# Kernel optimization log

Measured on AMD Instinct MI355X. Metric: run time of the kernel, lower is better.

The kernel has to match this reference:

```python
import jax, jax.numpy as jnp
import numpy as np

NUM_EMBEDDINGS = 1024
EMBEDDING_DIM = 64
COMMITMENT_COST = 0.25


def setup_inputs() -> dict:
    key = jax.random.key(0)
    k1, k2 = jax.random.split(key)
    latents = jax.random.normal(k1, (64, EMBEDDING_DIM, 32, 32), dtype=jnp.float32)
    # torch init: uniform_(-1/num_embeddings, 1/num_embeddings)
    codebook = jax.random.uniform(
        k2, (NUM_EMBEDDINGS, EMBEDDING_DIM), dtype=jnp.float32,
        minval=-1.0 / NUM_EMBEDDINGS, maxval=1.0 / NUM_EMBEDDINGS)
    return {"latents": latents, "codebook": codebook}


def reference(latents, codebook):
    B, C, H, W = latents.shape
    K = codebook.shape[0]
    x = jnp.transpose(latents, (0, 2, 3, 1))            # [B,H,W,C]
    x_flat = x.reshape(-1, C)                            # [N,C]
    # squared euclidean distances [N,K]
    dist = (jnp.sum(x_flat ** 2, axis=1, keepdims=True)
            + jnp.sum(codebook ** 2, axis=1)
            - 2.0 * x_flat @ codebook.T)
    idx = jnp.argmin(dist, axis=1)                       # [N] int
    q_flat = codebook[idx]                               # [N,C]
    q = q_flat.reshape(x.shape)                          # [B,H,W,C]
    e_loss = jnp.mean((jax.lax.stop_gradient(q) - x) ** 2)
    q_loss = jnp.mean((q - jax.lax.stop_gradient(x)) ** 2)
    vq_loss = q_loss + COMMITMENT_COST * e_loss
    # straight-through estimator
    q_st = x + jax.lax.stop_gradient(q - x)
    quantized = jnp.transpose(q_st, (0, 3, 1, 2))        # [B,C,H,W]
    # perplexity from code usage histogram
    N = x_flat.shape[0]
    avg_probs = jnp.zeros((K,), dtype=jnp.float32).at[idx].add(1.0) / N
    perplexity = jnp.exp(-jnp.sum(avg_probs * jnp.log(avg_probs + 1e-10)))
    encoding_indices = idx.reshape(B, H, W)
    return (vq_loss, quantized, perplexity, encoding_indices)
```

## Files before the change

### kernel.cpp

```cpp
#include <hip/hip_runtime.h>

#define N_PTS   65536
#define K_CODES 1024
#define C_DIM   64
#define HW      1024
#define Q_ELEMS 4194304

#define OUT_Q_OFF 1
#define OUT_P_OFF 4194305
#define OUT_I_OFF 4194306

#define WS_HIST 0
#define WS_SSE  4096
#define WS_CSUM 8192
#define WS_CBP  16384

#define EPS_A_W 7.5e-5f
#define EPS_T_W 2.0e-4f

typedef float f32x16 __attribute__((ext_vector_type(16)));
typedef short bf16x8 __attribute__((ext_vector_type(8)));

__device__ __forceinline__ unsigned short bf16rn(float f) {
    unsigned int u = __float_as_uint(f);
    return (unsigned short)((u + 0x7FFFu + ((u >> 16) & 1u)) >> 16);
}
__device__ __forceinline__ float bf16tof(unsigned short h) {
    return __uint_as_float(((unsigned int)h) << 16);
}

__device__ __forceinline__ float np_pairwise_sumsq64(const float* a) {
    float r[8];
    #pragma unroll
    for (int j = 0; j < 8; ++j) r[j] = __fmul_rn(a[j], a[j]);
    #pragma unroll
    for (int i = 8; i < 64; i += 8) {
        #pragma unroll
        for (int j = 0; j < 8; ++j)
            r[j] = __fadd_rn(r[j], __fmul_rn(a[i + j], a[i + j]));
    }
    return __fadd_rn(__fadd_rn(__fadd_rn(r[0], r[1]), __fadd_rn(r[2], r[3])),
                     __fadd_rn(__fadd_rn(r[4], r[5]), __fadd_rn(r[6], r[7])));
}

__global__ void vq_prep(const float* __restrict__ cb, float* __restrict__ csum,
                        unsigned short* __restrict__ cbp) {
    int g = blockIdx.x * 256 + threadIdx.x;
    int t = g >> 6, lane = g & 63, l31 = lane & 31, half = lane >> 5;
    int row = t * 32 + l31;
    const float* r = cb + row * 64;
    float cs = np_pairwise_sumsq64(r);
    if (half == 0) csum[row] = cs;
    size_t tb = (size_t)t * 9 * 512;
    #pragma unroll
    for (int c = 0; c < 4; ++c) {
        bf16x8 h8, l8;
        #pragma unroll
        for (int j = 0; j < 8; ++j) {
            float f = r[c * 16 + half * 8 + j];
            unsigned short h = bf16rn(f);
            h8[j] = (short)h;
            l8[j] = (short)bf16rn(f - bf16tof(h));
        }
        *(bf16x8*)(cbp + tb + (size_t)(c * 2 + 0) * 512 + lane * 8) = h8;
        *(bf16x8*)(cbp + tb + (size_t)(c * 2 + 1) * 512 + lane * 8) = l8;
    }
    bf16x8 c8;
    #pragma unroll
    for (int j = 0; j < 8; ++j) c8[j] = 0;
    if (half == 0) c8[0] = (short)bf16rn(-0.5f * cs);
    *(bf16x8*)(cbp + tb + (size_t)8 * 512 + lane * 8) = c8;
}

__global__ __launch_bounds__(256, 2) void vq_main(
        const float* __restrict__ latents,
        const float* __restrict__ cb,
        const float* __restrict__ csum,
        const unsigned short* __restrict__ cbp,
        unsigned int* __restrict__ hist,
        double* __restrict__ sse,
        float* __restrict__ out) {
    __shared__ float xs[128 * 65];
    __shared__ float tmax[32 * 128];
    __shared__ float m1f[128];
    __shared__ int   fk[128], ambig[128], acount;
    __shared__ double dred[128];

    const int tid  = threadIdx.x;
    const int lane = tid & 63, wave = tid >> 6;
    const int n0 = blockIdx.x * 128;
    const int b = n0 >> 10, hw0 = n0 & 1023;
    const float* xg = latents + (size_t)b * C_DIM * HW + hw0;

    for (int i = tid; i < 128 * 64; i += 256) {
        int p = i & 127, d = i >> 7;
        xs[p * 65 + d] = xg[(size_t)d * HW + p];
    }
    if (tid == 0) acount = 0;
    __syncthreads();

    const int l31 = lane & 31, half = lane >> 5;
    const int pb = (wave << 5) + l31;
    bf16x8 xh[4], xl[4], x4;
    #pragma unroll
    for (int c = 0; c < 4; ++c)
        #pragma unroll
        for (int j = 0; j < 8; ++j) {
            float f = xs[pb * 65 + c * 16 + half * 8 + j];
            unsigned short h = bf16rn(f);
            xh[c][j] = (short)h;
            xl[c][j] = (short)bf16rn(f - bf16tof(h));
        }
    #pragma unroll
    for (int j = 0; j < 8; ++j) x4[j] = 0;
    if (half == 0) x4[0] = (short)0x3F80;

    float m1 = -3e38f, m2 = -3e38f;
    int i1 = 0;
    const int RC[16] = {0,1,2,3,8,9,10,11,16,17,18,19,24,25,26,27};
    const int rh4 = half * 4;
    const bf16x8* base = (const bf16x8*)cbp;

    auto screen_tile = [&](int t, const bf16x8* ch, const bf16x8* cl, bf16x8 ca) {
        f32x16 accA, accB;
        #pragma unroll
        for (int r = 0; r < 16; ++r) { accA[r] = 0.0f; accB[r] = 0.0f; }
        #pragma unroll
        for (int c = 0; c < 4; ++c)
            accA = __builtin_amdgcn_mfma_f32_32x32x16_bf16(ch[c], xh[c], accA, 0, 0, 0);
        accA = __builtin_amdgcn_mfma_f32_32x32x16_bf16(ca, x4, accA, 0, 0, 0);
        #pragma unroll
        for (int c = 0; c < 4; ++c)
            accB = __builtin_amdgcn_mfma_f32_32x32x16_bf16(ch[c], xl[c], accB, 0, 0, 0);
        #pragma unroll
        for (int c = 0; c < 4; ++c)
            accB = __builtin_amdgcn_mfma_f32_32x32x16_bf16(cl[c], xh[c], accB, 0, 0, 0);
        float tl = -3e38f;
        const int tb = t << 5;
        #pragma unroll
        for (int r = 0; r < 16; ++r) {
            float v = accA[r] + accB[r];
            int k = tb + RC[r] + rh4;
            m2 = fmaxf(m2, fminf(m1, v));
            i1 = (v > m1) ? k : i1;
            m1 = fmaxf(m1, v);
            tl = fmaxf(tl, v);
        }
        tl = fmaxf(tl, __shfl_xor(tl, 32, 64));
        if (half == 0) tmax[t * 128 + pb] = tl;
    };
    auto load_tile = [&](int t, bf16x8* ch, bf16x8* cl, bf16x8& ca) {
        const bf16x8* bp = base + (size_t)t * 576 + lane;
        #pragma unroll
        for (int c = 0; c < 4; ++c) {
            ch[c] = bp[c * 128];
            cl[c] = bp[c * 128 + 64];
        }
        ca = bp[512];
    };

    bf16x8 chA[4], clA[4], caA, chB[4], clB[4], caB;
    load_tile(0, chA, clA, caA);
    for (int t = 0; t < 32; t += 2) {
        load_tile(t + 1, chB, clB, caB);
        screen_tile(t, chA, clA, caA);
        if (t + 2 < 32) load_tile(t + 2, chA, clA, caA);
        screen_tile(t + 1, chB, clB, caB);
    }
    {
        float m1o = __shfl_xor(m1, 32, 64);
        float m2o = __shfl_xor(m2, 32, 64);
        int   i1o = __shfl_xor(i1, 32, 64);
        m2 = fmaxf(fmaxf(m2, m2o), fminf(m1, m1o));
        i1 = (m1o > m1) ? i1o : i1;
        m1 = fmaxf(m1, m1o);
        if (half == 0) {
            m1f[pb] = m1;
            fk[pb] = i1;
            if (m2 >= m1 - EPS_A_W) {
                int a = atomicAdd(&acount, 1);
                ambig[a] = pb;
            }
        }
    }
    __syncthreads();

    for (int a = wave; a < acount; a += 4) {
        int p = ambig[a];
        const float* xrow = &xs[p * 65];
        float Aq = np_pairwise_sumsq64(xrow);
        float thr = m1f[p] - EPS_T_W;
        unsigned long long best = ~0ULL;
        for (int t = 0; t < 32; ++t) {
            if (tmax[t * 128 + p] < thr) continue;
            if (lane < 32) {
                int k = (t << 5) + lane;
                const float* crow = cb + (size_t)k * 64;
                float m = 0.0f;
                #pragma unroll
                for (int d = 0; d < 64; ++d) m = __fmaf_rn(xrow[d], crow[d], m);
                float D = __fsub_rn(__fadd_rn(Aq, csum[k]), __fmul_rn(2.0f, m));
                unsigned long long key =
                    ((unsigned long long)__float_as_uint(D) << 10) | (unsigned)k;
                best = (key < best) ? key : best;
            }
        }
        #pragma unroll
        for (int off = 32; off > 0; off >>= 1) {
            unsigned long long o = __shfl_xor(best, off, 64);
            best = (o < best) ? o : best;
        }
        if (lane == 0) fk[p] = (int)(best & 1023ULL);
    }
    __syncthreads();

    if (tid < 128) {
        int myk = fk[tid];
        out[OUT_I_OFF + n0 + tid] = (float)myk;
        atomicAdd(&hist[myk], 1u);
        const float* crow = cb + (size_t)myk * 64;
        const float* xrow = &xs[tid * 65];
        double e = 0.0;
        #pragma unroll
        for (int d = 0; d < 64; ++d) {
            double df = (double)xrow[d] - (double)crow[d];
            e = fma(df, df, e);
        }
        dred[tid] = e;
    }
    __syncthreads();
    if (tid < 64) {
        double v = dred[tid] + dred[tid + 64];
        #pragma unroll
        for (int off = 32; off > 0; off >>= 1) v += __shfl_down(v, off, 64);
        if (tid == 0) atomicAdd(sse, v);
    }
    for (int i = tid; i < 128 * 64; i += 256) {
        int p = i & 127, c = i >> 7;
        out[OUT_Q_OFF + (size_t)b * 65536 + (size_t)c * HW + hw0 + p] =
            cb[(size_t)fk[p] * 64 + c];
    }
}

__global__ void vq_final(const unsigned int* __restrict__ hist,
                         const double* __restrict__ sse,
                         float* __restrict__ out) {
    __shared__ double red[256];
    int t = threadIdx.x;
    double s = 0.0;
    for (int i = t; i < K_CODES; i += 256) {
        double p = (double)hist[i] / (double)N_PTS;
        s += p * log(p + 1e-10);
    }
    red[t] = s;
    __syncthreads();
    for (int w = 128; w > 0; w >>= 1) {
        if (t < w) red[t] += red[t + w];
        __syncthreads();
    }
    if (t == 0) {
        out[OUT_P_OFF] = (float)exp(-red[0]);
        out[0] = (float)(1.25 * sse[0] / (double)Q_ELEMS);
    }
}

extern "C" void kernel_launch(void* const* d_in, const int* in_sizes, int n_in,
                              void* d_out, int out_size, void* d_ws, size_t ws_size,
                              hipStream_t stream) {
    const float* latents = (const float*)d_in[0];
    const float* cb      = (const float*)d_in[1];
    float* out = (float*)d_out;
    char* ws = (char*)d_ws;

    unsigned int*   hist = (unsigned int*)(ws + WS_HIST);
    double*         sse  = (double*)(ws + WS_SSE);
    float*          csum = (float*)(ws + WS_CSUM);
    unsigned short* cbp  = (unsigned short*)(ws + WS_CBP);

    hipMemsetAsync(ws, 0, 4096 + 8, stream);

    vq_prep <<<8, 256, 0, stream>>>(cb, csum, cbp);
    vq_main <<<N_PTS / 128, 256, 0, stream>>>(latents, cb, csum, cbp, hist, sse, out);
    vq_final<<<1, 256, 0, stream>>>(hist, sse, out);
}
```

Baseline: 141.2 us.

## Split codebook across wave pairs, halve block size, fuse final reduction into main kernel

The main kernel now handles 64 points per block, and wave pairs split the 32 codebook tiles between them. Their partial top-2 results are merged through shared memory, which doubles the block count and raises the occupancy hint to 3 blocks per CU. The separate finalize kernel is replaced by a last-block-done counter, so one launch is removed. The codebook prep kernel is restaged through LDS with more blocks for coalesced reads. In exchange, the explicit double-buffered tile prefetch is dropped, and each point adds a cross-wave merge plus a shared-memory sync.

Result: slower. 157.3 us (+11.4%).

```diff
diff --git a/kernel.cpp b/kernel.cpp
--- a/kernel.cpp
+++ b/kernel.cpp
@@ -5,15 +5,17 @@
 #define C_DIM   64
 #define HW      1024
 #define Q_ELEMS 4194304
+#define NBLOCKS 1024
 
 #define OUT_Q_OFF 1
 #define OUT_P_OFF 4194305
 #define OUT_I_OFF 4194306
 
 #define WS_HIST 0
-#define WS_SSE  4096
-#define WS_CSUM 8192
-#define WS_CBP  16384
+#define WS_CNT  4096
+#define WS_SSE  4104
+#define WS_CSUM 4112
+#define WS_CBP  8208
 
 #define EPS_A_W 7.5e-5f
 #define EPS_T_W 2.0e-4f
@@ -45,62 +47,80 @@
 
 __global__ void vq_prep(const float* __restrict__ cb, float* __restrict__ csum,
                         unsigned short* __restrict__ cbp) {
-    int g = blockIdx.x * 256 + threadIdx.x;
-    int t = g >> 6, lane = g & 63, l31 = lane & 31, half = lane >> 5;
-    int row = t * 32 + l31;
-    const float* r = cb + row * 64;
-    float cs = np_pairwise_sumsq64(r);
-    if (half == 0) csum[row] = cs;
-    size_t tb = (size_t)t * 9 * 512;
-    #pragma unroll
-    for (int c = 0; c < 4; ++c) {
-        bf16x8 h8, l8;
-        #pragma unroll
-        for (int j = 0; j < 8; ++j) {
-            float f = r[c * 16 + half * 8 + j];
-            unsigned short h = bf16rn(f);
-            h8[j] = (short)h;
-            l8[j] = (short)bf16rn(f - bf16tof(h));
-        }
-        *(bf16x8*)(cbp + tb + (size_t)(c * 2 + 0) * 512 + lane * 8) = h8;
-        *(bf16x8*)(cbp + tb + (size_t)(c * 2 + 1) * 512 + lane * 8) = l8;
-    }
-    bf16x8 c8;
-    #pragma unroll
-    for (int j = 0; j < 8; ++j) c8[j] = 0;
-    if (half == 0) c8[0] = (short)bf16rn(-0.5f * cs);
-    *(bf16x8*)(cbp + tb + (size_t)8 * 512 + lane * 8) = c8;
-}
-
-__global__ __launch_bounds__(256, 2) void vq_main(
+    __shared__ float rs[32 * 65];
+    __shared__ float csl[32];
+    const int t = blockIdx.x, tid = threadIdx.x;
+    const float* src = cb + (size_t)t * 2048;
+    for (int i = tid; i < 2048; i += 256) {
+        int row = i >> 6, d = i & 63;
+        rs[row * 65 + d] = src[i];
+    }
+    __syncthreads();
+    if (tid < 32) {
+        float cs = np_pairwise_sumsq64(&rs[tid * 65]);
+        csum[t * 32 + tid] = cs;
+        csl[tid] = cs;
+    }
+    __syncthreads();
+    if (tid < 64) {
+        int l31 = tid & 31, half = tid >> 5;
+        const float* r = &rs[l31 * 65];
+        unsigned short* dst = cbp + (size_t)t * 9 * 512;
+        #pragma unroll
+        for (int c = 0; c < 4; ++c) {
+            bf16x8 h8, l8;
+            #pragma unroll
+            for (int j = 0; j < 8; ++j) {
+                float f = r[c * 16 + half * 8 + j];
+                unsigned short h = bf16rn(f);
+                h8[j] = (short)h;
+                l8[j] = (short)bf16rn(f - bf16tof(h));
+            }
+            *(bf16x8*)(dst + (size_t)(c * 2 + 0) * 512 + tid * 8) = h8;
+            *(bf16x8*)(dst + (size_t)(c * 2 + 1) * 512 + tid * 8) = l8;
+        }
+        bf16x8 c8;
+        #pragma unroll
+        for (int j = 0; j < 8; ++j) c8[j] = 0;
+        if (half == 0) c8[0] = (short)bf16rn(-0.5f * csl[l31]);
+        *(bf16x8*)(dst + (size_t)8 * 512 + tid * 8) = c8;
+    }
+}
+
+__global__ __launch_bounds__(256, 3) void vq_main(
         const float* __restrict__ latents,
         const float* __restrict__ cb,
         const float* __restrict__ csum,
         const unsigned short* __restrict__ cbp,
         unsigned int* __restrict__ hist,
         double* __restrict__ sse,
+        unsigned int* __restrict__ counter,
         float* __restrict__ out) {
-    __shared__ float xs[128 * 65];
-    __shared__ float tmax[32 * 128];
-    __shared__ float m1f[128];
-    __shared__ int   fk[128], ambig[128], acount;
-    __shared__ double dred[128];
+    __shared__ float xs[64 * 65];
+    __shared__ float tmax[32 * 64];
+    __shared__ float sm1[2][64], sm2[2][64];
+    __shared__ int   si1[2][64];
+    __shared__ float m1f[64];
+    __shared__ int   fk[64], ambig[64];
+    __shared__ int   acount, lastflag;
+    __shared__ double red[256];
 
     const int tid  = threadIdx.x;
     const int lane = tid & 63, wave = tid >> 6;
-    const int n0 = blockIdx.x * 128;
+    const int chh = wave & 1, pg = wave >> 1;
+    const int n0 = blockIdx.x * 64;
     const int b = n0 >> 10, hw0 = n0 & 1023;
     const float* xg = latents + (size_t)b * C_DIM * HW + hw0;
 
-    for (int i = tid; i < 128 * 64; i += 256) {
-        int p = i & 127, d = i >> 7;
+    for (int i = tid; i < 64 * 64; i += 256) {
+        int p = i & 63, d = i >> 6;
         xs[p * 65 + d] = xg[(size_t)d * HW + p];
     }
     if (tid == 0) acount = 0;
     __syncthreads();
 
     const int l31 = lane & 31, half = lane >> 5;
-    const int pb = (wave << 5) + l31;
+    const int pb = (pg << 5) + l31;
     bf16x8 xh[4], xl[4], x4;
     #pragma unroll
     for (int c = 0; c < 4; ++c)
@@ -119,53 +139,43 @@
     int i1 = 0;
     const int RC[16] = {0,1,2,3,8,9,10,11,16,17,18,19,24,25,26,27};
     const int rh4 = half * 4;
-    const bf16x8* base = (const bf16x8*)cbp;
-
-    auto screen_tile = [&](int t, const bf16x8* ch, const bf16x8* cl, bf16x8 ca) {
-        f32x16 accA, accB;
-        #pragma unroll
-        for (int r = 0; r < 16; ++r) { accA[r] = 0.0f; accB[r] = 0.0f; }
+
+    for (int t = 0; t < 16; ++t) {
+        const int tg = (chh << 4) + t;
+        const bf16x8* bp = (const bf16x8*)cbp + (size_t)tg * 576 + lane;
+        bf16x8 ch[4], cl[4], ca;
+        #pragma unroll
+        for (int c = 0; c < 4; ++c) {
+            ch[c] = bp[c * 128];
+            cl[c] = bp[c * 128 + 64];
+        }
+        ca = bp[512];
+        f32x16 accA, accB1, accB2;
+        #pragma unroll
+        for (int r = 0; r < 16; ++r) { accA[r] = 0.0f; accB1[r] = 0.0f; accB2[r] = 0.0f; }
         #pragma unroll
         for (int c = 0; c < 4; ++c)
             accA = __builtin_amdgcn_mfma_f32_32x32x16_bf16(ch[c], xh[c], accA, 0, 0, 0);
         accA = __builtin_amdgcn_mfma_f32_32x32x16_bf16(ca, x4, accA, 0, 0, 0);
         #pragma unroll
         for (int c = 0; c < 4; ++c)
-            accB = __builtin_amdgcn_mfma_f32_32x32x16_bf16(ch[c], xl[c], accB, 0, 0, 0);
+            accB1 = __builtin_amdgcn_mfma_f32_32x32x16_bf16(ch[c], xl[c], accB1, 0, 0, 0);
         #pragma unroll
         for (int c = 0; c < 4; ++c)
-            accB = __builtin_amdgcn_mfma_f32_32x32x16_bf16(cl[c], xh[c], accB, 0, 0, 0);
+            accB2 = __builtin_amdgcn_mfma_f32_32x32x16_bf16(cl[c], xh[c], accB2, 0, 0, 0);
         float tl = -3e38f;
-        const int tb = t << 5;
+        const int tb2 = tg << 5;
         #pragma unroll
         for (int r = 0; r < 16; ++r) {
-            float v = accA[r] + accB[r];
-            int k = tb + RC[r] + rh4;
+            float v = __fadd_rn(__fadd_rn(accA[r], accB1[r]), accB2[r]);
+            int k = tb2 + RC[r] + rh4;
             m2 = fmaxf(m2, fminf(m1, v));
             i1 = (v > m1) ? k : i1;
             m1 = fmaxf(m1, v);
             tl = fmaxf(tl, v);
         }
         tl = fmaxf(tl, __shfl_xor(tl, 32, 64));
-        if (half == 0) tmax[t * 128 + pb] = tl;
-    };
-    auto load_tile = [&](int t, bf16x8* ch, bf16x8* cl, bf16x8& ca) {
-        const bf16x8* bp = base + (size_t)t * 576 + lane;
-        #pragma unroll
-        for (int c = 0; c < 4; ++c) {
-            ch[c] = bp[c * 128];
-            cl[c] = bp[c * 128 + 64];
-        }
-        ca = bp[512];
-    };
-
-    bf16x8 chA[4], clA[4], caA, chB[4], clB[4], caB;
-    load_tile(0, chA, clA, caA);
-    for (int t = 0; t < 32; t += 2) {
-        load_tile(t + 1, chB, clB, caB);
-        screen_tile(t, chA, clA, caA);
-        if (t + 2 < 32) load_tile(t + 2, chA, clA, caA);
-        screen_tile(t + 1, chB, clB, caB);
+        if (half == 0) tmax[tg * 64 + pb] = tl;
     }
     {
         float m1o = __shfl_xor(m1, 32, 64);
@@ -174,13 +184,20 @@
         m2 = fmaxf(fmaxf(m2, m2o), fminf(m1, m1o));
         i1 = (m1o > m1) ? i1o : i1;
         m1 = fmaxf(m1, m1o);
-        if (half == 0) {
-            m1f[pb] = m1;
-            fk[pb] = i1;
-            if (m2 >= m1 - EPS_A_W) {
-                int a = atomicAdd(&acount, 1);
-                ambig[a] = pb;
-            }
+        if (half == 0) { sm1[chh][pb] = m1; sm2[chh][pb] = m2; si1[chh][pb] = i1; }
+    }
+    __syncthreads();
+
+    if (tid < 64) {
+        float a1 = sm1[0][tid], a2 = sm2[0][tid];
+        float b1 = sm1[1][tid], b2 = sm2[1][tid];
+        float mm1 = fmaxf(a1, b1);
+        float mm2 = fmaxf(fminf(a1, b1), fmaxf(a2, b2));
+        m1f[tid] = mm1;
+        fk[tid] = (b1 > a1) ? si1[1][tid] : si1[0][tid];
+        if (mm2 >= mm1 - EPS_A_W) {
+            int a = atomicAdd(&acount, 1);
+            ambig[a] = tid;
         }
     }
     __syncthreads();
@@ -192,7 +209,7 @@
         float thr = m1f[p] - EPS_T_W;
         unsigned long long best = ~0ULL;
         for (int t = 0; t < 32; ++t) {
-            if (tmax[t * 128 + p] < thr) continue;
+            if (tmax[t * 64 + p] < thr) continue;
             if (lane < 32) {
                 int k = (t << 5) + lane;
                 const float* crow = cb + (size_t)k * 64;
@@ -214,7 +231,7 @@
     }
     __syncthreads();
 
-    if (tid < 128) {
+    if (tid < 64) {
         int myk = fk[tid];
         out[OUT_I_OFF + n0 + tid] = (float)myk;
         atomicAdd(&hist[myk], 1u);
@@ -226,41 +243,36 @@
             double df = (double)xrow[d] - (double)crow[d];
             e = fma(df, df, e);
         }
-        dred[tid] = e;
-    }
-    __syncthreads();
-    if (tid < 64) {
-        double v = dred[tid] + dred[tid + 64];
-        #pragma unroll
-        for (int off = 32; off > 0; off >>= 1) v += __shfl_down(v, off, 64);
-        if (tid == 0) atomicAdd(sse, v);
-    }
-    for (int i = tid; i < 128 * 64; i += 256) {
-        int p = i & 127, c = i >> 7;
+        #pragma unroll
+        for (int off = 32; off > 0; off >>= 1) e += __shfl_down(e, off, 64);
+        if (tid == 0) atomicAdd(sse, e);
+    }
+    for (int i = tid; i < 64 * 64; i += 256) {
+        int p = i & 63, c = i >> 6;
         out[OUT_Q_OFF + (size_t)b * 65536 + (size_t)c * HW + hw0 + p] =
             cb[(size_t)fk[p] * 64 + c];
     }
-}
-
-__global__ void vq_final(const unsigned int* __restrict__ hist,
-                         const double* __restrict__ sse,
-                         float* __restrict__ out) {
-    __shared__ double red[256];
-    int t = threadIdx.x;
-    double s = 0.0;
-    for (int i = t; i < K_CODES; i += 256) {
-        double p = (double)hist[i] / (double)N_PTS;
-        s += p * log(p + 1e-10);
-    }
-    red[t] = s;
-    __syncthreads();
-    for (int w = 128; w > 0; w >>= 1) {
-        if (t < w) red[t] += red[t + w];
+
+    __syncthreads();
+    if (tid == 0) lastflag = (atomicAdd(counter, 1u) == NBLOCKS - 1) ? 1 : 0;
+    __syncthreads();
+    if (lastflag) {
+        double s = 0.0;
+        for (int i = tid; i < K_CODES; i += 256) {
+            double p = (double)atomicAdd(&hist[i], 0u) / (double)N_PTS;
+            s += p * log(p + 1e-10);
+        }
+        red[tid] = s;
         __syncthreads();
-    }
-    if (t == 0) {
-        out[OUT_P_OFF] = (float)exp(-red[0]);
-        out[0] = (float)(1.25 * sse[0] / (double)Q_ELEMS);
+        for (int w = 128; w > 0; w >>= 1) {
+            if (tid < w) red[tid] += red[tid + w];
+            __syncthreads();
+        }
+        if (tid == 0) {
+            out[OUT_P_OFF] = (float)exp(-red[0]);
+            double sv = atomicAdd(sse, 0.0);
+            out[0] = (float)(1.25 * sv / (double)Q_ELEMS);
+        }
     }
 }
 
@@ -272,14 +284,14 @@
     float* out = (float*)d_out;
     char* ws = (char*)d_ws;
 
-    unsigned int*   hist = (unsigned int*)(ws + WS_HIST);
-    double*         sse  = (double*)(ws + WS_SSE);
-    float*          csum = (float*)(ws + WS_CSUM);
-    unsigned short* cbp  = (unsigned short*)(ws + WS_CBP);
-
-    hipMemsetAsync(ws, 0, 4096 + 8, stream);
-
-    vq_prep <<<8, 256, 0, stream>>>(cb, csum, cbp);
-    vq_main <<<N_PTS / 128, 256, 0, stream>>>(latents, cb, csum, cbp, hist, sse, out);
-    vq_final<<<1, 256, 0, stream>>>(hist, sse, out);
-}
+    unsigned int*   hist    = (unsigned int*)(ws + WS_HIST);
+    unsigned int*   counter = (unsigned int*)(ws + WS_CNT);
+    double*         sse     = (double*)(ws + WS_SSE);
+    float*          csum    = (float*)(ws + WS_CSUM);
+    unsigned short* cbp     = (unsigned short*)(ws + WS_CBP);
+
+    hipMemsetAsync(ws, 0, 4112, stream);
+
+    vq_prep <<<32, 256, 0, stream>>>(cb, csum, cbp);
+    vq_main <<<NBLOCKS, 256, 0, stream>>>(latents, cb, csum, cbp, hist, sse, counter, out);
+}
```

## Fold zeroing into prep and finalize in last block to drop launches

Applied to the files above, without the earlier changes.

Removes the hipMemsetAsync and the separate final kernel. Zeroing of the histogram, counter and SSE now happens inside the prep kernel, and the last vq_main block to finish, found through an atomic counter, computes perplexity and loss. The prep kernel is also rebuilt to stage codebook rows through shared memory across 32 blocks, and one add is made explicitly round-to-nearest. This saves two launch and dependency gaps, at the cost of an atomic-counter handshake whose memory ordering between blocks relies on atomic reads.

Result: no change. 142.8 us (+1.1%).

```diff
diff --git a/kernel.cpp b/kernel.cpp
--- a/kernel.cpp
+++ b/kernel.cpp
@@ -5,15 +5,17 @@
 #define C_DIM   64
 #define HW      1024
 #define Q_ELEMS 4194304
+#define NBLOCKS 512
 
 #define OUT_Q_OFF 1
 #define OUT_P_OFF 4194305
 #define OUT_I_OFF 4194306
 
 #define WS_HIST 0
-#define WS_SSE  4096
-#define WS_CSUM 8192
-#define WS_CBP  16384
+#define WS_CNT  4096
+#define WS_SSE  4104
+#define WS_CSUM 4112
+#define WS_CBP  8208
 
 #define EPS_A_W 7.5e-5f
 #define EPS_T_W 2.0e-4f
@@ -44,32 +46,46 @@
 }
 
 __global__ void vq_prep(const float* __restrict__ cb, float* __restrict__ csum,
-                        unsigned short* __restrict__ cbp) {
-    int g = blockIdx.x * 256 + threadIdx.x;
-    int t = g >> 6, lane = g & 63, l31 = lane & 31, half = lane >> 5;
-    int row = t * 32 + l31;
-    const float* r = cb + row * 64;
-    float cs = np_pairwise_sumsq64(r);
-    if (half == 0) csum[row] = cs;
-    size_t tb = (size_t)t * 9 * 512;
-    #pragma unroll
-    for (int c = 0; c < 4; ++c) {
-        bf16x8 h8, l8;
-        #pragma unroll
-        for (int j = 0; j < 8; ++j) {
-            float f = r[c * 16 + half * 8 + j];
-            unsigned short h = bf16rn(f);
-            h8[j] = (short)h;
-            l8[j] = (short)bf16rn(f - bf16tof(h));
-        }
-        *(bf16x8*)(cbp + tb + (size_t)(c * 2 + 0) * 512 + lane * 8) = h8;
-        *(bf16x8*)(cbp + tb + (size_t)(c * 2 + 1) * 512 + lane * 8) = l8;
-    }
-    bf16x8 c8;
-    #pragma unroll
-    for (int j = 0; j < 8; ++j) c8[j] = 0;
-    if (half == 0) c8[0] = (short)bf16rn(-0.5f * cs);
-    *(bf16x8*)(cbp + tb + (size_t)8 * 512 + lane * 8) = c8;
+                        unsigned short* __restrict__ cbp,
+                        unsigned int* __restrict__ hist,
+                        unsigned int* __restrict__ counter,
+                        double* __restrict__ sse) {
+    __shared__ float rs[32 * 65];
+    __shared__ float csl[32];
+    const int t = blockIdx.x, tid = threadIdx.x;
+    if (tid < 32) hist[t * 32 + tid] = 0u;
+    if (t == 0 && tid == 0) { *counter = 0u; *sse = 0.0; }
+    const float* src = cb + (size_t)t * 2048;
+    for (int i = tid; i < 2048; i += 256) {
+        int row = i >> 6, d = i & 63;
+        rs[row * 65 + d] = src[i];
+    }
+    __syncthreads();
+    if (tid < 32) {
+        float cs = np_pairwise_sumsq64(&rs[tid * 65]);
+        csum[t * 32 + tid] = cs;
+        csl[tid] = cs;
+    }
+    __syncthreads();
+    for (int u = tid; u < 576; u += 256) {
+        int s = u >> 6, lane = u & 63, l31 = lane & 31, half = lane >> 5;
+        bf16x8 v8;
+        if (s < 8) {
+            int c = s >> 1, lo = s & 1;
+            const float* r = &rs[l31 * 65 + c * 16 + half * 8];
+            #pragma unroll
+            for (int j = 0; j < 8; ++j) {
+                float f = r[j];
+                unsigned short h = bf16rn(f);
+                v8[j] = lo ? (short)bf16rn(f - bf16tof(h)) : (short)h;
+            }
+        } else {
+            #pragma unroll
+            for (int j = 0; j < 8; ++j) v8[j] = 0;
+            if (half == 0) v8[0] = (short)bf16rn(-0.5f * csl[l31]);
+        }
+        *(bf16x8*)(cbp + (size_t)t * 4608 + (size_t)s * 512 + lane * 8) = v8;
+    }
 }
 
 __global__ __launch_bounds__(256, 2) void vq_main(
@@ -79,12 +95,14 @@
         const unsigned short* __restrict__ cbp,
         unsigned int* __restrict__ hist,
         double* __restrict__ sse,
+        unsigned int* __restrict__ counter,
         float* __restrict__ out) {
     __shared__ float xs[128 * 65];
     __shared__ float tmax[32 * 128];
     __shared__ float m1f[128];
     __shared__ int   fk[128], ambig[128], acount;
-    __shared__ double dred[128];
+    __shared__ int   lastflag;
+    __shared__ double red[256];
 
     const int tid  = threadIdx.x;
     const int lane = tid & 63, wave = tid >> 6;
@@ -139,7 +157,7 @@
         const int tb = t << 5;
         #pragma unroll
         for (int r = 0; r < 16; ++r) {
-            float v = accA[r] + accB[r];
+            float v = __fadd_rn(accA[r], accB[r]);
             int k = tb + RC[r] + rh4;
             m2 = fmaxf(m2, fminf(m1, v));
             i1 = (v > m1) ? k : i1;
@@ -226,11 +244,11 @@
             double df = (double)xrow[d] - (double)crow[d];
             e = fma(df, df, e);
         }
-        dred[tid] = e;
+        red[tid] = e;
     }
     __syncthreads();
     if (tid < 64) {
-        double v = dred[tid] + dred[tid + 64];
+        double v = red[tid] + red[tid + 64];
         #pragma unroll
         for (int off = 32; off > 0; off >>= 1) v += __shfl_down(v, off, 64);
         if (tid == 0) atomicAdd(sse, v);
@@ -240,27 +258,27 @@
         out[OUT_Q_OFF + (size_t)b * 65536 + (size_t)c * HW + hw0 + p] =
             cb[(size_t)fk[p] * 64 + c];
     }
-}
-
-__global__ void vq_final(const unsigned int* __restrict__ hist,
-                         const double* __restrict__ sse,
-                         float* __restrict__ out) {
-    __shared__ double red[256];
-    int t = threadIdx.x;
-    double s = 0.0;
-    for (int i = t; i < K_CODES; i += 256) {
-        double p = (double)hist[i] / (double)N_PTS;
-        s += p * log(p + 1e-10);
-    }
-    red[t] = s;
-    __syncthreads();
-    for (int w = 128; w > 0; w >>= 1) {
-        if (t < w) red[t] += red[t + w];
+
+    __syncthreads();
+    if (tid == 0) lastflag = (atomicAdd(counter, 1u) == NBLOCKS - 1) ? 1 : 0;
+    __syncthreads();
+    if (lastflag) {
+        double s = 0.0;
+        for (int i = tid; i < K_CODES; i += 256) {
+            double p = (double)atomicAdd(&hist[i], 0u) / (double)N_PTS;
+            s += p * log(p + 1e-10);
+        }
+        red[tid] = s;
         __syncthreads();
-    }
-    if (t == 0) {
-        out[OUT_P_OFF] = (float)exp(-red[0]);
-        out[0] = (float)(1.25 * sse[0] / (double)Q_ELEMS);
+        for (int w = 128; w > 0; w >>= 1) {
+            if (tid < w) red[tid] += red[tid + w];
+            __syncthreads();
+        }
+        if (tid == 0) {
+            out[OUT_P_OFF] = (float)exp(-red[0]);
+            double sv = atomicAdd(sse, 0.0);
+            out[0] = (float)(1.25 * sv / (double)Q_ELEMS);
+        }
     }
 }
 
@@ -272,14 +290,12 @@
     float* out = (float*)d_out;
     char* ws = (char*)d_ws;
 
-    unsigned int*   hist = (unsigned int*)(ws + WS_HIST);
-    double*         sse  = (double*)(ws + WS_SSE);
-    float*          csum = (float*)(ws + WS_CSUM);
-    unsigned short* cbp  = (unsigned short*)(ws + WS_CBP);
-
-    hipMemsetAsync(ws, 0, 4096 + 8, stream);
-
-    vq_prep <<<8, 256, 0, stream>>>(cb, csum, cbp);
-    vq_main <<<N_PTS / 128, 256, 0, stream>>>(latents, cb, csum, cbp, hist, sse, out);
-    vq_final<<<1, 256, 0, stream>>>(hist, sse, out);
-}
+    unsigned int*   hist    = (unsigned int*)(ws + WS_HIST);
+    unsigned int*   counter = (unsigned int*)(ws + WS_CNT);
+    double*         sse     = (double*)(ws + WS_SSE);
+    float*          csum    = (float*)(ws + WS_CSUM);
+    unsigned short* cbp     = (unsigned short*)(ws + WS_CBP);
+
+    vq_prep <<<32, 256, 0, stream>>>(cb, csum, cbp, hist, counter, sse);
+    vq_main <<<NBLOCKS, 256, 0, stream>>>(latents, cb, csum, cbp, hist, sse, counter, out);
+}
```
